# Performance work log

Hardware: AMD Instinct MI355X
Metric: run time of the kernel (lower is better)

The kernel has to match this reference:

```python
import jax, jax.numpy as jnp
import numpy as np

ALPHA = 0.1  # config['alpha']


def setup_inputs() -> dict:
    key = jax.random.key(0)
    k1, k2, k3, k4, k5 = jax.random.split(key, 5)
    n_bs, bit, n_cls, class_bit, n_train = 128, 48, 100, 16, 10000
    u = jax.random.normal(k1, (n_bs, bit), dtype=jnp.float32)
    # multi-hot labels (float, as in torch: y.float())
    y = jax.random.bernoulli(k2, 0.1, (n_bs, n_cls)).astype(jnp.float32)
    ind = jnp.arange(n_bs, dtype=jnp.int64)  # distinct in-range row indices
    # buffers mid-training: U holds previous class-wise codes, Y previous labels
    U = jax.random.normal(k3, (n_train, n_cls, class_bit), dtype=jnp.float32) * 0.1
    Y = jax.random.bernoulli(k4, 0.1, (n_train, n_cls)).astype(jnp.float32)
    # xavier_uniform-like init for w_D [n_class, bit, class_bit]
    limit = np.sqrt(6.0 / (bit + class_bit)).astype(np.float32)
    w_D = jax.random.uniform(k5, (n_cls, bit, class_bit), dtype=jnp.float32,
                             minval=-limit, maxval=limit)
    return {"u": u, "y": y, "ind": ind, "U": U, "Y": Y, "w_D": w_D}


def reference(u, y, ind, U, Y, w_D):
    # update label buffer: self.Y[ind, :] = y
    Y = Y.at[ind].set(y)
    # u_ = matmul(u, w_D).permute(1,0,2): [n_bs, n_cls, class_bit]
    u_ = jnp.einsum('bk,ckd->bcd', u, w_D)
    # update code buffer with detached u_ (torch: self.U[ind] = u_.data)
    U = U.at[ind].set(jax.lax.stop_gradient(u_))
    # pairwise similarity s: [n_bs, n_train, n_cls]
    s = y[:, None, :] * Y[None, :, :]
    # inner_product: sum over class_bit -> [n_bs, n_train, n_cls]
    ip = jnp.einsum('tcd,bcd->btc', U, u_)
    # stable log(1 + exp(ip)) - s*ip, exactly as the torch expression
    likelihood = (jnp.log1p(jnp.exp(-jnp.abs(ip))) + jnp.maximum(ip, 0.0)
                  - s * ip).mean()
    quantization = ALPHA * jnp.mean((u_ - jnp.sign(u_)) ** 2)
    return likelihood + quantization
```

## Files before the change

kernel.cpp:

```cpp
#include <hip/hip_runtime.h>
#include <math.h>

#define CB 16
#define ALPHA 0.1f
#define LOG2E 1.4426950408889634f
#define LN2F  0.6931471805599453f
#define MAXW 8
#define N_BS 128
#define BIT  48
#define UPAD 52

typedef __bf16 bf16x8 __attribute__((ext_vector_type(8)));
typedef float  f32x16 __attribute__((ext_vector_type(16)));

__global__ __launch_bounds__(256, 4) void loss_fused(
        const float* __restrict__ u, const float* __restrict__ y,
        const float* __restrict__ w_D,
        const float* __restrict__ U, const float* __restrict__ Yb,
        const int* __restrict__ ind,
        float* __restrict__ partials, float* __restrict__ quant_partials,
        int n_cls, int n_train, int ntile, int GY) {
    __shared__ float smf[N_BS * UPAD + 4 * BIT * CB];
    __shared__ int pflag[MAXW * 32];
    float* u_lds   = smf;
    float* wd_lds  = smf + N_BS * UPAD;
    float* u_slice = smf;

    const int tid  = threadIdx.x;
    const int lane = tid & 63;
    const int wid  = tid >> 6;
    const int bx   = blockIdx.x;
    const int by   = blockIdx.y;
    const int c    = bx * 4 + wid;
    const int r    = lane & 31;
    const int h    = lane >> 5;
    const int nw   = (ntile - by + GY - 1) / GY;

    pflag[tid] = -1;
    #pragma unroll
    for (int it = 0; it < N_BS * (BIT / 4) / 256; ++it) {
        int f = it * 256 + tid;
        int b = f / (BIT / 4), k4 = f % (BIT / 4);
        *(float4*)&u_lds[b * UPAD + k4 * 4] =
            *(const float4*)&u[(size_t)b * BIT + k4 * 4];
    }
    #pragma unroll
    for (int it = 0; it < 4 * BIT * (CB / 4) / 256; ++it) {
        int f = it * 256 + tid;
        int cc = f / (BIT * CB / 4), rest = f % (BIT * CB / 4);
        *(float4*)&wd_lds[cc * BIT * CB + rest * 4] =
            *(const float4*)&w_D[(size_t)(bx * 4 + cc) * BIT * CB + rest * 4];
    }
    __syncthreads();

    if (tid < N_BS) {
        int t = ind[tid];
        for (int w = 0; w < nw; ++w) {
            unsigned rl = (unsigned)(t - (by + w * GY) * 32);
            if (rl < 32u) pflag[w * 32 + rl] = tid;
        }
    }

    float acc0[8] = {0,0,0,0,0,0,0,0};
    float acc1[8] = {0,0,0,0,0,0,0,0};
    float acc2[8] = {0,0,0,0,0,0,0,0};
    float acc3[8] = {0,0,0,0,0,0,0,0};
    {
        const float* __restrict__ wdc = wd_lds + wid * BIT * CB + h * 8;
        for (int k4 = 0; k4 < BIT / 4; ++k4) {
            float4 ub0 = *(const float4*)&u_lds[(0 * 32 + r) * UPAD + k4 * 4];
            float4 ub1 = *(const float4*)&u_lds[(1 * 32 + r) * UPAD + k4 * 4];
            float4 ub2 = *(const float4*)&u_lds[(2 * 32 + r) * UPAD + k4 * 4];
            float4 ub3 = *(const float4*)&u_lds[(3 * 32 + r) * UPAD + k4 * 4];
            #pragma unroll
            for (int kk = 0; kk < 4; ++kk) {
                const float* wrow = wdc + (k4 * 4 + kk) * CB;
                float w8[8];
                float4 wa = *(const float4*)(wrow);
                float4 wb = *(const float4*)(wrow + 4);
                w8[0]=wa.x; w8[1]=wa.y; w8[2]=wa.z; w8[3]=wa.w;
                w8[4]=wb.x; w8[5]=wb.y; w8[6]=wb.z; w8[7]=wb.w;
                float s0 = (&ub0.x)[kk], s1 = (&ub1.x)[kk];
                float s2 = (&ub2.x)[kk], s3 = (&ub3.x)[kk];
                #pragma unroll
                for (int j = 0; j < 8; ++j) {
                    acc0[j] = fmaf(s0, w8[j], acc0[j]);
                    acc1[j] = fmaf(s1, w8[j], acc1[j]);
                    acc2[j] = fmaf(s2, w8[j], acc2[j]);
                    acc3[j] = fmaf(s3, w8[j], acc3[j]);
                }
            }
        }
    }

    if (by == 0) {
        float q = 0.f;
        #pragma unroll
        for (int j = 0; j < 8; ++j) {
            float v, sgn, d;
            v = acc0[j]; sgn = (v>0.f)?1.f:((v<0.f)?-1.f:0.f); d = v-sgn; q = fmaf(d,d,q);
            v = acc1[j]; sgn = (v>0.f)?1.f:((v<0.f)?-1.f:0.f); d = v-sgn; q = fmaf(d,d,q);
            v = acc2[j]; sgn = (v>0.f)?1.f:((v<0.f)?-1.f:0.f); d = v-sgn; q = fmaf(d,d,q);
            v = acc3[j]; sgn = (v>0.f)?1.f:((v<0.f)?-1.f:0.f); d = v-sgn; q = fmaf(d,d,q);
        }
        #pragma unroll
        for (int off = 32; off > 0; off >>= 1) q += __shfl_down(q, off, 64);
        if (lane == 0) quant_partials[bx * 4 + wid] = q;
    }

    float ypc0 = y[(size_t)(0 * 32 + r) * n_cls + c];
    float ypc1 = y[(size_t)(1 * 32 + r) * n_cls + c];
    float ypc2 = y[(size_t)(2 * 32 + r) * n_cls + c];
    float ypc3 = y[(size_t)(3 * 32 + r) * n_cls + c];
    float vv[8], ww[8];
    #pragma unroll
    for (int j = 0; j < 8; ++j) {
        ww[j] = acc0[j] + acc1[j] + acc2[j] + acc3[j];
        vv[j] = ypc0*acc0[j] + ypc1*acc1[j] + ypc2*acc2[j] + ypc3*acc3[j];
    }
    #pragma unroll
    for (int m = 1; m < 32; m <<= 1) {
        #pragma unroll
        for (int j = 0; j < 8; ++j) {
            vv[j] += __shfl_xor(vv[j], m, 64);
            ww[j] += __shfl_xor(ww[j], m, 64);
        }
    }

    bf16x8 B0, B1, B2, B3;
    #pragma unroll
    for (int j = 0; j < 8; ++j) {
        B0[j] = (__bf16)(acc0[j] * LOG2E);
        B1[j] = (__bf16)(acc1[j] * LOG2E);
        B2[j] = (__bf16)(acc2[j] * LOG2E);
        B3[j] = (__bf16)(acc3[j] * LOG2E);
    }

    __syncthreads();
    {
        float* dst = u_slice + wid * N_BS * CB + r * CB + h * 8;
        *(float4*)(dst + 0*32*CB)     = make_float4(acc0[0],acc0[1],acc0[2],acc0[3]);
        *(float4*)(dst + 0*32*CB + 4) = make_float4(acc0[4],acc0[5],acc0[6],acc0[7]);
        *(float4*)(dst + 1*32*CB)     = make_float4(acc1[0],acc1[1],acc1[2],acc1[3]);
        *(float4*)(dst + 1*32*CB + 4) = make_float4(acc1[4],acc1[5],acc1[6],acc1[7]);
        *(float4*)(dst + 2*32*CB)     = make_float4(acc2[0],acc2[1],acc2[2],acc2[3]);
        *(float4*)(dst + 2*32*CB + 4) = make_float4(acc2[4],acc2[5],acc2[6],acc2[7]);
        *(float4*)(dst + 3*32*CB)     = make_float4(acc3[0],acc3[1],acc3[2],acc3[3]);
        *(float4*)(dst + 3*32*CB + 4) = make_float4(acc3[4],acc3[5],acc3[6],acc3[7]);
    }
    __syncthreads();

    float acc = 0.f;
    f32x16 zc = {};
    int rc0 = by * 32 + r;
    if (rc0 >= n_train) rc0 = n_train - 1;
    const float* __restrict__ ar0 = U + ((size_t)rc0 * n_cls + c) * CB + h * 8;
    float4 a0c = *(const float4*)(ar0);
    float4 a1c = *(const float4*)(ar0 + 4);
    float  Yvc = Yb[(size_t)rc0 * n_cls + c];

    #pragma unroll 1
    for (int w = 0; w < nw; ++w) {
        float4 a0n = a0c, a1n = a1c; float Yvn = Yvc;
        if (w + 1 < nw) {
            int rcn = (by + (w + 1) * GY) * 32 + r;
            if (rcn >= n_train) rcn = n_train - 1;
            const float* __restrict__ arn =
                U + ((size_t)rcn * n_cls + c) * CB + h * 8;
            a0n = *(const float4*)(arn);
            a1n = *(const float4*)(arn + 4);
            Yvn = Yb[(size_t)rcn * n_cls + c];
        }

        const int t0  = (by + w * GY) * 32;
        const int row = t0 + r;
        const int pf  = pflag[w * 32 + r];
        if (pf >= 0) {
            const float* src = u_slice + wid * N_BS * CB + pf * CB + h * 8;
            a0c = *(const float4*)(src);
            a1c = *(const float4*)(src + 4);
            Yvc = y[(size_t)pf * n_cls + c];
        }
        if (row >= n_train) {
            a0c = make_float4(0.f, 0.f, 0.f, 0.f); a1c = a0c; Yvc = 0.f;
        }

        float sv = a0c.x*vv[0] + a0c.y*vv[1] + a0c.z*vv[2] + a0c.w*vv[3]
                 + a1c.x*vv[4] + a1c.y*vv[5] + a1c.z*vv[6] + a1c.w*vv[7];
        float sw = a0c.x*ww[0] + a0c.y*ww[1] + a0c.z*ww[2] + a0c.w*ww[3]
                 + a1c.x*ww[4] + a1c.y*ww[5] + a1c.z*ww[6] + a1c.w*ww[7];

        bf16x8 A;
        A[0] = (__bf16)a0c.x; A[1] = (__bf16)a0c.y;
        A[2] = (__bf16)a0c.z; A[3] = (__bf16)a0c.w;
        A[4] = (__bf16)a1c.x; A[5] = (__bf16)a1c.y;
        A[6] = (__bf16)a1c.z; A[7] = (__bf16)a1c.w;

        float accA = 0.f;
        float pp   = 1.f;
        #pragma unroll
        for (int bt = 0; bt < 4; ++bt) {
            bf16x8 Bf = (bt == 0) ? B0 : (bt == 1) ? B1 : (bt == 2) ? B2 : B3;
            f32x16 D = __builtin_amdgcn_mfma_f32_32x32x16_bf16(A, Bf, zc,
                                                               0, 0, 0);
            float a[16];
            #pragma unroll
            for (int j = 0; j < 16; ++j) {
                float ipa = fabsf(D[j]);
                a[j] = 1.0f + __builtin_amdgcn_exp2f(-ipa);
                accA += ipa;
            }
            #pragma unroll
            for (int s = 1; s < 16; s <<= 1)
                #pragma unroll
                for (int j = 0; j < 16; j += 2 * s) a[j] *= a[j + s];
            pp *= a[0];
        }
        float accL = __builtin_amdgcn_logf(pp);
        acc += LN2F * accL + (0.5f * LN2F) * accA + 0.5f * sw - Yvc * sv;

        a0c = a0n; a1c = a1n; Yvc = Yvn;
    }

    #pragma unroll
    for (int off = 32; off > 0; off >>= 1)
        acc += __shfl_down(acc, off, 64);
    if (lane == 0) {
        int bid = by * gridDim.x + bx;
        partials[bid * 4 + wid] = acc;
    }
}

__global__ __launch_bounds__(256) void finalize_kernel(
        const float* __restrict__ partials, int nblk,
        const float* __restrict__ quant_partials, int n_quant,
        float* __restrict__ out, double pad_corr,
        double like_scale, double quant_scale) {
    double s = 0.0, q = 0.0;
    for (int i = threadIdx.x; i < nblk; i += 256) s += (double)partials[i];
    for (int i = threadIdx.x; i < n_quant; i += 256) q += (double)quant_partials[i];
    #pragma unroll
    for (int off = 32; off > 0; off >>= 1) {
        s += __shfl_down(s, off, 64);
        q += __shfl_down(q, off, 64);
    }
    __shared__ double dred[4][2];
    int lane = threadIdx.x & 63, wid = threadIdx.x >> 6;
    if (lane == 0) { dred[wid][0] = s; dred[wid][1] = q; }
    __syncthreads();
    if (threadIdx.x == 0) {
        double S = dred[0][0] + dred[1][0] + dred[2][0] + dred[3][0];
        double Q = dred[0][1] + dred[1][1] + dred[2][1] + dred[3][1];
        out[0] = (float)((S - pad_corr) * like_scale + Q * quant_scale);
    }
}

extern "C" void kernel_launch(void* const* d_in, const int* in_sizes, int n_in,
                              void* d_out, int out_size, void* d_ws, size_t ws_size,
                              hipStream_t stream) {
    const float* u   = (const float*)d_in[0];
    const float* y   = (const float*)d_in[1];
    const int*   ind = (const int*)d_in[2];
    const float* U   = (const float*)d_in[3];
    const float* Yb  = (const float*)d_in[4];
    const float* w_D = (const float*)d_in[5];

    const int n_bs    = in_sizes[2];
    const int n_cls   = in_sizes[1] / n_bs;
    const int n_train = in_sizes[4] / n_cls;

    const int totalU = n_bs * n_cls * CB;
    const int ntile  = (n_train + 31) / 32;
    const int GY     = (ntile + MAXW - 1) / MAXW;
    const int gx     = (n_cls + 3) / 4;
    const int nblk   = GY * gx;
    const int npart  = nblk * 4;
    const int nquant = gx * 4;

    char* ws = (char*)d_ws;
    size_t off = 0;
    float* partials = (float*)(ws + off);        off += (size_t)npart * 4;
    float* quant_partials = (float*)(ws + off);  off += (size_t)nquant * 4;

    loss_fused<<<dim3(gx, GY), 256, 0, stream>>>(
        u, y, w_D, U, Yb, ind, partials, quant_partials,
        n_cls, n_train, ntile, GY);

    const double ln2 = 0.6931471805599453;
    const double n_pad = (double)((long long)(GY * MAXW * 32 - n_train) *
                                  (long long)n_bs * (long long)n_cls);
    const double pad_corr    = ln2 * n_pad;
    const double like_scale  = 1.0 / ((double)n_bs * n_train * n_cls);
    const double quant_scale = (double)ALPHA / (double)totalU;

    finalize_kernel<<<1, 256, 0, stream>>>(partials, npart,
                                           quant_partials, nquant,
                                           (float*)d_out, pad_corr,
                                           like_scale, quant_scale);
}
```

Baseline: 48.78 us.

## Shrink LDS footprint: read w_D from global, store u_ slice as bf16, raise grid size

Drops the LDS staging of w_D and reads weights directly from global memory in the projection loop. The per-wave u_ slice used for overwritten rows is now stored in LDS as packed bf16 with a padded stride of 9 words, and is unpacked when a row matches. Together these cut shared memory per block, which should allow more resident blocks. MAXW drops from 8 to 5, so GY and the grid grow, and the padding correction now uses ntile*32. The cost is extra precision loss on the substituted rows and global loads for the weights.

```diff
diff --git a/kernel.cpp b/kernel.cpp
--- a/kernel.cpp
+++ b/kernel.cpp
@@ -5,13 +5,18 @@
 #define ALPHA 0.1f
 #define LOG2E 1.4426950408889634f
 #define LN2F  0.6931471805599453f
-#define MAXW 8
+#define MAXW 5
 #define N_BS 128
 #define BIT  48
 #define UPAD 52
 
 typedef __bf16 bf16x8 __attribute__((ext_vector_type(8)));
 typedef float  f32x16 __attribute__((ext_vector_type(16)));
+
+__device__ __forceinline__ unsigned int f2bf(float x) {
+    unsigned int v = __float_as_uint(x);
+    return (v + 0x7FFFu + ((v >> 16) & 1u)) >> 16;
+}
 
 __global__ __launch_bounds__(256, 4) void loss_fused(
         const float* __restrict__ u, const float* __restrict__ y,
@@ -20,11 +25,10 @@
         const int* __restrict__ ind,
         float* __restrict__ partials, float* __restrict__ quant_partials,
         int n_cls, int n_train, int ntile, int GY) {
-    __shared__ float smf[N_BS * UPAD + 4 * BIT * CB];
+    __shared__ float smf[N_BS * UPAD];
     __shared__ int pflag[MAXW * 32];
-    float* u_lds   = smf;
-    float* wd_lds  = smf + N_BS * UPAD;
-    float* u_slice = smf;
+    float* u_lds = smf;
+    unsigned int* ubf32 = (unsigned int*)smf;
 
     const int tid  = threadIdx.x;
     const int lane = tid & 63;
@@ -36,7 +40,7 @@
     const int h    = lane >> 5;
     const int nw   = (ntile - by + GY - 1) / GY;
 
-    pflag[tid] = -1;
+    if (tid < MAXW * 32) pflag[tid] = -1;
     #pragma unroll
     for (int it = 0; it < N_BS * (BIT / 4) / 256; ++it) {
         int f = it * 256 + tid;
@@ -44,13 +48,6 @@
         *(float4*)&u_lds[b * UPAD + k4 * 4] =
             *(const float4*)&u[(size_t)b * BIT + k4 * 4];
     }
-    #pragma unroll
-    for (int it = 0; it < 4 * BIT * (CB / 4) / 256; ++it) {
-        int f = it * 256 + tid;
-        int cc = f / (BIT * CB / 4), rest = f % (BIT * CB / 4);
-        *(float4*)&wd_lds[cc * BIT * CB + rest * 4] =
-            *(const float4*)&w_D[(size_t)(bx * 4 + cc) * BIT * CB + rest * 4];
-    }
     __syncthreads();
 
     if (tid < N_BS) {
@@ -66,7 +63,7 @@
     float acc2[8] = {0,0,0,0,0,0,0,0};
     float acc3[8] = {0,0,0,0,0,0,0,0};
     {
-        const float* __restrict__ wdc = wd_lds + wid * BIT * CB + h * 8;
+        const float* __restrict__ wdc = w_D + (size_t)c * BIT * CB + h * 8;
         for (int k4 = 0; k4 < BIT / 4; ++k4) {
             float4 ub0 = *(const float4*)&u_lds[(0 * 32 + r) * UPAD + k4 * 4];
             float4 ub1 = *(const float4*)&u_lds[(1 * 32 + r) * UPAD + k4 * 4];
@@ -75,9 +72,9 @@
             #pragma unroll
             for (int kk = 0; kk < 4; ++kk) {
                 const float* wrow = wdc + (k4 * 4 + kk) * CB;
-                float w8[8];
                 float4 wa = *(const float4*)(wrow);
                 float4 wb = *(const float4*)(wrow + 4);
+                float w8[8];
                 w8[0]=wa.x; w8[1]=wa.y; w8[2]=wa.z; w8[3]=wa.w;
                 w8[4]=wb.x; w8[5]=wb.y; w8[6]=wb.z; w8[7]=wb.w;
                 float s0 = (&ub0.x)[kk], s1 = (&ub1.x)[kk];
@@ -138,15 +135,17 @@
 
     __syncthreads();
     {
-        float* dst = u_slice + wid * N_BS * CB + r * CB + h * 8;
-        *(float4*)(dst + 0*32*CB)     = make_float4(acc0[0],acc0[1],acc0[2],acc0[3]);
-        *(float4*)(dst + 0*32*CB + 4) = make_float4(acc0[4],acc0[5],acc0[6],acc0[7]);
-        *(float4*)(dst + 1*32*CB)     = make_float4(acc1[0],acc1[1],acc1[2],acc1[3]);
-        *(float4*)(dst + 1*32*CB + 4) = make_float4(acc1[4],acc1[5],acc1[6],acc1[7]);
-        *(float4*)(dst + 2*32*CB)     = make_float4(acc2[0],acc2[1],acc2[2],acc2[3]);
-        *(float4*)(dst + 2*32*CB + 4) = make_float4(acc2[4],acc2[5],acc2[6],acc2[7]);
-        *(float4*)(dst + 3*32*CB)     = make_float4(acc3[0],acc3[1],acc3[2],acc3[3]);
-        *(float4*)(dst + 3*32*CB + 4) = make_float4(acc3[4],acc3[5],acc3[6],acc3[7]);
+        unsigned int* d0 = &ubf32[(wid * N_BS + 0 * 32 + r) * 9 + h * 4];
+        unsigned int* d1 = &ubf32[(wid * N_BS + 1 * 32 + r) * 9 + h * 4];
+        unsigned int* d2 = &ubf32[(wid * N_BS + 2 * 32 + r) * 9 + h * 4];
+        unsigned int* d3 = &ubf32[(wid * N_BS + 3 * 32 + r) * 9 + h * 4];
+        #pragma unroll
+        for (int j2 = 0; j2 < 4; ++j2) {
+            d0[j2] = f2bf(acc0[2*j2]) | (f2bf(acc0[2*j2+1]) << 16);
+            d1[j2] = f2bf(acc1[2*j2]) | (f2bf(acc1[2*j2+1]) << 16);
+            d2[j2] = f2bf(acc2[2*j2]) | (f2bf(acc2[2*j2+1]) << 16);
+            d3[j2] = f2bf(acc3[2*j2]) | (f2bf(acc3[2*j2+1]) << 16);
+        }
     }
     __syncthreads();
 
@@ -176,9 +175,16 @@
         const int row = t0 + r;
         const int pf  = pflag[w * 32 + r];
         if (pf >= 0) {
-            const float* src = u_slice + wid * N_BS * CB + pf * CB + h * 8;
-            a0c = *(const float4*)(src);
-            a1c = *(const float4*)(src + 4);
+            const unsigned int* src = &ubf32[(wid * N_BS + pf) * 9 + h * 4];
+            unsigned int w0 = src[0], w1 = src[1], w2 = src[2], w3 = src[3];
+            a0c.x = __uint_as_float(w0 << 16);
+            a0c.y = __uint_as_float(w0 & 0xFFFF0000u);
+            a0c.z = __uint_as_float(w1 << 16);
+            a0c.w = __uint_as_float(w1 & 0xFFFF0000u);
+            a1c.x = __uint_as_float(w2 << 16);
+            a1c.y = __uint_as_float(w2 & 0xFFFF0000u);
+            a1c.z = __uint_as_float(w3 << 16);
+            a1c.w = __uint_as_float(w3 & 0xFFFF0000u);
             Yvc = y[(size_t)pf * n_cls + c];
         }
         if (row >= n_train) {
@@ -287,7 +293,7 @@
         n_cls, n_train, ntile, GY);
 
     const double ln2 = 0.6931471805599453;
-    const double n_pad = (double)((long long)(GY * MAXW * 32 - n_train) *
+    const double n_pad = (double)((long long)(ntile * 32 - n_train) *
                                   (long long)n_bs * (long long)n_cls);
     const double pad_corr    = ln2 * n_pad;
     const double like_scale  = 1.0 / ((double)n_bs * n_train * n_cls);
```

Result: slower. 67.66 us (+38.7%).
